# Kernel tuning notes

Measured on AMD Instinct MI355X. Metric: run time of the kernel, lower is better.

## Reference

```python
import jax, jax.numpy as jnp
import numpy as np

B, L, V, D = 16384, 50, 1000000, 128

def setup_inputs() -> dict:
    key = jax.random.key(0)
    k1, k2, k3, k4, k5, k6 = jax.random.split(key, 6)
    entities = jax.random.randint(k1, (B,), 0, V, dtype=jnp.int64)
    history = jax.random.randint(k2, (B, L), 0, V, dtype=jnp.int64)
    hist_len = jax.random.randint(k3, (B,), 0, L + 1, dtype=jnp.int64)
    entities_emb = jax.random.normal(k4, (V, D), dtype=jnp.float32)
    # LinearQ parameters (torch nn.Linear: y = x @ W.T + b)
    bound = 1.0 / np.sqrt(D)
    W = jax.random.uniform(k5, (D, D), minval=-bound, maxval=bound, dtype=jnp.float32)
    b = jax.random.uniform(k6, (D,), minval=-bound, maxval=bound, dtype=jnp.float32)
    return {"entities": entities, "history": history, "hist_len": hist_len,
            "entities_emb": entities_emb, "W": W, "b": b}

def reference(entities, history, hist_len, entities_emb, W, b):
    # Gather history embeddings: [B, L, D]; mask out padding past hist_len.
    # Original code SUMS history embeddings (the torch.mean over a [1,D]
    # tensor is a no-op), so we sum masked gathers.
    mask = (jnp.arange(L)[None, :] < hist_len[:, None]).astype(entities_emb.dtype)  # [B, L]
    hist_emb = entities_emb[history]                       # [B, L, D]
    summed = jnp.einsum('bld,bl->bd', hist_emb, mask)       # [B, D]
    # Empty history -> fall back to the entity's own embedding.
    own = entities_emb[entities]                            # [B, D]
    his = jnp.where((hist_len == 0)[:, None], own, summed)  # [B, D]
    return his @ W.T + b                                    # [B, D]
```

## Files before the change

### kernel.cpp

```cpp
#include <hip/hip_runtime.h>

#define B_SZ 16384
#define L_SZ 50
#define D_SZ 128

__global__ void transpose_w_kernel(const float* __restrict__ W,
                                   float* __restrict__ WT) {
    int t = blockIdx.x * 256 + threadIdx.x;
    int j = t >> 7;
    int k = t & 127;
    WT[k * D_SZ + j] = W[j * D_SZ + k];
}

__global__ __launch_bounds__(256) void fused_event_emb_kernel(
    const int* __restrict__ entities,
    const int* __restrict__ history,
    const int* __restrict__ hist_len,
    const float* __restrict__ emb,
    const float* __restrict__ WT,
    const float* __restrict__ bias,
    float* __restrict__ out,
    int total_waves) {
    const int lane = threadIdx.x & 63;
    const int wave = __builtin_amdgcn_readfirstlane((int)(threadIdx.x >> 6));
    const int gwave = blockIdx.x * 4 + wave;

    const float2* emb2 = (const float2*)emb;
    const float2* wt2  = (const float2*)WT;
    const float2* b2   = (const float2*)bias;
    float2* out2       = (float2*)out;

    for (int r = gwave; r < B_SZ; r += total_waves) {
        const int hl = __builtin_amdgcn_readfirstlane(hist_len[r]);

        float2 acc = make_float2(0.0f, 0.0f);
        if (hl == 0) {
            const int e = entities[r];
            acc = emb2[(size_t)e * 64 + lane];
        } else {
            const int* hrow = history + r * L_SZ;
            int l = 0;
            for (; l + 4 <= hl; l += 4) {
                const int i0 = hrow[l + 0];
                const int i1 = hrow[l + 1];
                const int i2 = hrow[l + 2];
                const int i3 = hrow[l + 3];
                float2 v0 = emb2[(size_t)i0 * 64 + lane];
                float2 v1 = emb2[(size_t)i1 * 64 + lane];
                float2 v2 = emb2[(size_t)i2 * 64 + lane];
                float2 v3 = emb2[(size_t)i3 * 64 + lane];
                acc.x += (v0.x + v1.x) + (v2.x + v3.x);
                acc.y += (v0.y + v1.y) + (v2.y + v3.y);
            }
            for (; l < hl; ++l) {
                const int i0 = hrow[l];
                float2 v0 = emb2[(size_t)i0 * 64 + lane];
                acc.x += v0.x;
                acc.y += v0.y;
            }
        }

        float2 o = b2[lane];
        const unsigned sx = __float_as_uint(acc.x);
        const unsigned sy = __float_as_uint(acc.y);
#pragma unroll
        for (int k = 0; k < D_SZ; ++k) {
            const unsigned su =
                __builtin_amdgcn_readlane((k & 1) ? sy : sx, k >> 1);
            const float sk = __uint_as_float(su);
            const float2 w = wt2[k * 64 + lane];
            o.x = fmaf(sk, w.x, o.x);
            o.y = fmaf(sk, w.y, o.y);
        }
        out2[(size_t)r * 64 + lane] = o;
    }
}

extern "C" void kernel_launch(void* const* d_in, const int* in_sizes, int n_in,
                              void* d_out, int out_size, void* d_ws,
                              size_t ws_size, hipStream_t stream) {
    const int* entities   = (const int*)d_in[0];
    const int* history    = (const int*)d_in[1];
    const int* hist_len   = (const int*)d_in[2];
    const float* emb      = (const float*)d_in[3];
    const float* W        = (const float*)d_in[4];
    const float* bias     = (const float*)d_in[5];

    float* WT = (float*)d_ws;

    transpose_w_kernel<<<64, 256, 0, stream>>>(W, WT);

    const int blocks = 2048;
    const int total_waves = blocks * 4;
    fused_event_emb_kernel<<<blocks, 256, 0, stream>>>(
        entities, history, hist_len, emb, WT, bias, (float*)d_out, total_waves);
}
```

Before: 732.9 us.

## Fuse W transpose into LDS staging and process two rows per wave

Drops the separate transpose kernel and has each 1024-thread block load W transposed into a 64KB swizzled LDS tile. The 128x128 matvec then reads weights from LDS instead of global/L2. Each wave now handles exactly two rows and shares each weight load across both outputs. The costs are a per-block 64KB LDS fill, which limits occupancy to about two blocks per CU, plus a fixed grid/row mapping that depends on B.

```diff
diff --git a/kernel.cpp b/kernel.cpp
--- a/kernel.cpp
+++ b/kernel.cpp
@@ -3,40 +3,51 @@
 #define B_SZ 16384
 #define L_SZ 50
 #define D_SZ 128
+#define BLOCK_THREADS 1024
+#define WAVES_PER_BLOCK 16
+#define GRID_BLOCKS 512
+#define TOTAL_WAVES (GRID_BLOCKS * WAVES_PER_BLOCK)
 
-__global__ void transpose_w_kernel(const float* __restrict__ W,
-                                   float* __restrict__ WT) {
-    int t = blockIdx.x * 256 + threadIdx.x;
-    int j = t >> 7;
-    int k = t & 127;
-    WT[k * D_SZ + j] = W[j * D_SZ + k];
-}
-
-__global__ __launch_bounds__(256) void fused_event_emb_kernel(
+__global__ __launch_bounds__(BLOCK_THREADS, 8) void fused_event_emb_kernel(
     const int* __restrict__ entities,
     const int* __restrict__ history,
     const int* __restrict__ hist_len,
     const float* __restrict__ emb,
-    const float* __restrict__ WT,
+    const float* __restrict__ W,
     const float* __restrict__ bias,
-    float* __restrict__ out,
-    int total_waves) {
-    const int lane = threadIdx.x & 63;
-    const int wave = __builtin_amdgcn_readfirstlane((int)(threadIdx.x >> 6));
-    const int gwave = blockIdx.x * 4 + wave;
+    float* __restrict__ out) {
+    __shared__ float wt_lds[D_SZ * D_SZ];
+
+    const int tid = threadIdx.x;
+
+#pragma unroll
+    for (int i = 0; i < (D_SZ * D_SZ) / BLOCK_THREADS; ++i) {
+        const int idx = i * BLOCK_THREADS + tid;
+        const int j = idx >> 7;
+        const int k = idx & 127;
+        wt_lds[(k << 7) | (j ^ ((2 * k) & 62))] = W[idx];
+    }
+    __syncthreads();
+
+    const int lane = tid & 63;
+    const int wave = __builtin_amdgcn_readfirstlane(tid >> 6);
+    const int gw = blockIdx.x * WAVES_PER_BLOCK + wave;
 
     const float2* emb2 = (const float2*)emb;
-    const float2* wt2  = (const float2*)WT;
     const float2* b2   = (const float2*)bias;
     float2* out2       = (float2*)out;
 
-    for (int r = gwave; r < B_SZ; r += total_waves) {
+    const int r0 = gw;
+    const int r1 = gw + TOTAL_WAVES;
+
+    float2 acc0, acc1;
+#pragma unroll
+    for (int rr = 0; rr < 2; ++rr) {
+        const int r = (rr == 0) ? r0 : r1;
         const int hl = __builtin_amdgcn_readfirstlane(hist_len[r]);
-
-        float2 acc = make_float2(0.0f, 0.0f);
+        float2 a = make_float2(0.0f, 0.0f);
         if (hl == 0) {
-            const int e = entities[r];
-            acc = emb2[(size_t)e * 64 + lane];
+            a = emb2[(size_t)entities[r] * 64 + lane];
         } else {
             const int* hrow = history + r * L_SZ;
             int l = 0;
@@ -49,49 +60,60 @@
                 float2 v1 = emb2[(size_t)i1 * 64 + lane];
                 float2 v2 = emb2[(size_t)i2 * 64 + lane];
                 float2 v3 = emb2[(size_t)i3 * 64 + lane];
-                acc.x += (v0.x + v1.x) + (v2.x + v3.x);
-                acc.y += (v0.y + v1.y) + (v2.y + v3.y);
+                a.x += (v0.x + v1.x) + (v2.x + v3.x);
+                a.y += (v0.y + v1.y) + (v2.y + v3.y);
             }
             for (; l < hl; ++l) {
-                const int i0 = hrow[l];
-                float2 v0 = emb2[(size_t)i0 * 64 + lane];
-                acc.x += v0.x;
-                acc.y += v0.y;
+                float2 v = emb2[(size_t)hrow[l] * 64 + lane];
+                a.x += v.x;
+                a.y += v.y;
             }
         }
+        if (rr == 0) acc0 = a; else acc1 = a;
+    }
 
-        float2 o = b2[lane];
-        const unsigned sx = __float_as_uint(acc.x);
-        const unsigned sy = __float_as_uint(acc.y);
-#pragma unroll
-        for (int k = 0; k < D_SZ; ++k) {
-            const unsigned su =
-                __builtin_amdgcn_readlane((k & 1) ? sy : sx, k >> 1);
-            const float sk = __uint_as_float(su);
-            const float2 w = wt2[k * 64 + lane];
-            o.x = fmaf(sk, w.x, o.x);
-            o.y = fmaf(sk, w.y, o.y);
-        }
-        out2[(size_t)r * 64 + lane] = o;
+    float2 oa = b2[lane];
+    float2 ob = oa;
+    const int j0 = lane << 1;
+#pragma unroll 4
+    for (int k2 = 0; k2 < 64; ++k2) {
+        const int ke = 2 * k2;
+        const int ko = 2 * k2 + 1;
+        const float sa0 = __uint_as_float(
+            __builtin_amdgcn_readlane(__float_as_uint(acc0.x), k2));
+        const float sa1 = __uint_as_float(
+            __builtin_amdgcn_readlane(__float_as_uint(acc0.y), k2));
+        const float sb0 = __uint_as_float(
+            __builtin_amdgcn_readlane(__float_as_uint(acc1.x), k2));
+        const float sb1 = __uint_as_float(
+            __builtin_amdgcn_readlane(__float_as_uint(acc1.y), k2));
+        const float2 w0 =
+            *(const float2*)&wt_lds[(ke << 7) | (j0 ^ ((2 * ke) & 62))];
+        const float2 w1 =
+            *(const float2*)&wt_lds[(ko << 7) | (j0 ^ ((2 * ko) & 62))];
+        oa.x = fmaf(sa0, w0.x, oa.x);
+        oa.y = fmaf(sa0, w0.y, oa.y);
+        oa.x = fmaf(sa1, w1.x, oa.x);
+        oa.y = fmaf(sa1, w1.y, oa.y);
+        ob.x = fmaf(sb0, w0.x, ob.x);
+        ob.y = fmaf(sb0, w0.y, ob.y);
+        ob.x = fmaf(sb1, w1.x, ob.x);
+        ob.y = fmaf(sb1, w1.y, ob.y);
     }
+    out2[(size_t)r0 * 64 + lane] = oa;
+    out2[(size_t)r1 * 64 + lane] = ob;
 }
 
 extern "C" void kernel_launch(void* const* d_in, const int* in_sizes, int n_in,
                               void* d_out, int out_size, void* d_ws,
                               size_t ws_size, hipStream_t stream) {
-    const int* entities   = (const int*)d_in[0];
-    const int* history    = (const int*)d_in[1];
-    const int* hist_len   = (const int*)d_in[2];
-    const float* emb      = (const float*)d_in[3];
-    const float* W        = (const float*)d_in[4];
-    const float* bias     = (const float*)d_in[5];
+    const int* entities = (const int*)d_in[0];
+    const int* history  = (const int*)d_in[1];
+    const int* hist_len = (const int*)d_in[2];
+    const float* emb    = (const float*)d_in[3];
+    const float* W      = (const float*)d_in[4];
+    const float* bias   = (const float*)d_in[5];
 
-    float* WT = (float*)d_ws;
-
-    transpose_w_kernel<<<64, 256, 0, stream>>>(W, WT);
-
-    const int blocks = 2048;
-    const int total_waves = blocks * 4;
-    fused_event_emb_kernel<<<blocks, 256, 0, stream>>>(
-        entities, history, hist_len, emb, WT, bias, (float*)d_out, total_waves);
+    fused_event_emb_kernel<<<GRID_BLOCKS, BLOCK_THREADS, 0, stream>>>(
+        entities, history, hist_len, emb, W, bias, (float*)d_out);
 }
```

Result: faster. 611.4 us (-16.6%).
